# Kernel optimization log

Hardware: AMD Instinct MI355X
Metric: run time of the kernel (lower is better)

Reference implementation:

```python
import jax, jax.numpy as jnp
import numpy as np

N = 131072
K = 1024
D = 64

def setup_inputs() -> dict:
    key = jax.random.key(0)
    k1, k2 = jax.random.split(key)
    x = jax.random.normal(k1, (N, D), dtype=jnp.float32)
    emb_weight = jax.random.normal(k2, (K, D), dtype=jnp.float32)
    return {"x": x, "emb_weight": emb_weight}

def reference(x, emb_weight):
    distances = (
        jnp.sum(x * x, axis=1, keepdims=True)
        + jnp.sum(emb_weight * emb_weight, axis=1)
        - 2.0 * jnp.matmul(x, emb_weight.T)
    )
    codebook_indices = jnp.argmin(distances, axis=1)  # [N]
    probs = jax.nn.one_hot(codebook_indices, K, dtype=x.dtype)  # [N, K]
    z_q = emb_weight[codebook_indices]  # [N, D]
    return (z_q, probs)
```

## Files before the change

kernel.cpp:

```cpp
#include <hip/hip_runtime.h>
#include <math.h>

#define N_TOK 131072
#define K_CB  1024
#define D_DIM 64
#define MARGIN_U 72u

#define WS_EN     0
#define WS_ES     4096
#define WS_CNT    266240
#define WS_LIST   266256

typedef short bf16x8 __attribute__((ext_vector_type(8)));
typedef float f32x4  __attribute__((ext_vector_type(4)));

__device__ __forceinline__ ushort f2bf(float f) {
    uint u = __float_as_uint(f);
    u += 0x7FFFu + ((u >> 16) & 1u);
    return (ushort)(u >> 16);
}
__device__ __forceinline__ float bf2f(ushort h) {
    return __uint_as_float(((uint)h) << 16);
}

__global__ __launch_bounds__(256) void prep_kernel(
    const float* __restrict__ emb, float* __restrict__ en,
    ushort* __restrict__ es, uint* __restrict__ fixcnt)
{
    const int tid = threadIdx.x;
    const int pb  = blockIdx.x;
    const int c6  = tid & 63;
    const int q   = tid >> 6;
    const int code = pb * 64 + c6;
    if (pb == 0 && tid == 0) *fixcnt = 0;

    const int cb = code >> 4, jj = code & 15;
    const float* er = emb + (size_t)code * D_DIM;
    #pragma unroll
    for (int j = 0; j < 16; ++j) {
        int d = q * 16 + j;
        float f = er[d];
        ushort h = f2bf(f);
        ushort l = f2bf(f - bf2f(h));
        int ks = d >> 5, quad = (d >> 3) & 3, e = d & 7;
        es[(size_t)(((cb * 4 + ks)     * 4 + quad) * 16 + jj) * 8 + e] = h;
        es[(size_t)(((cb * 4 + ks + 2) * 4 + quad) * 16 + jj) * 8 + e] = l;
    }
    if (q == 0) {
        float s = 0.f;
        #pragma unroll
        for (int d = 0; d < D_DIM; ++d) s = fmaf(er[d], er[d], s);
        en[code] = s;
    }
}

__global__ __launch_bounds__(256) void vq_onehot(
    const float* __restrict__ x, const float* __restrict__ emb,
    const float* __restrict__ en, const ushort* __restrict__ es,
    float* __restrict__ zq, float* __restrict__ probs,
    uint* __restrict__ fixcnt, uint* __restrict__ fixlist, uint fixcap)
{
    const int tid  = threadIdx.x;
    const int wave = tid >> 6, lane = tid & 63;
    const int quad = lane >> 4, l15 = lane & 15;
    const int rg = wave >> 1;
    const int h  = wave & 1;
    const int blockRow = blockIdx.x * 64;
    const int waveRowBase = blockRow + rg * 32;

    __shared__ uint lds_b1[2][64];
    __shared__ uint lds_b2[2][64];
    __shared__ int  lds_bk[64];

    bf16x8 af[2][4];
    #pragma unroll
    for (int g = 0; g < 2; ++g) {
        const float* xr = x + (size_t)(waveRowBase + g * 16 + l15) * D_DIM + quad * 8;
        f32x4 p0 = *(const f32x4*)(xr);
        f32x4 p1 = *(const f32x4*)(xr + 4);
        f32x4 p2 = *(const f32x4*)(xr + 32);
        f32x4 p3 = *(const f32x4*)(xr + 36);
        float v0[8], v1[8];
        #pragma unroll
        for (int j = 0; j < 4; ++j) { v0[j] = p0[j]; v0[4 + j] = p1[j]; v1[j] = p2[j]; v1[4 + j] = p3[j]; }
        #pragma unroll
        for (int j = 0; j < 8; ++j) {
            ushort h0 = f2bf(v0[j]);
            af[g][0][j] = (short)h0;
            af[g][2][j] = (short)f2bf(v0[j] - bf2f(h0));
            ushort h1 = f2bf(v1[j]);
            af[g][1][j] = (short)h1;
            af[g][3][j] = (short)f2bf(v1[j] - bf2f(h1));
        }
    }

    uint b1u[8], b2u[8];
    #pragma unroll
    for (int s = 0; s < 8; ++s) { b1u[s] = 0xFFFFFFFFu; b2u[s] = 0xFFFFFFFFu; }

    const bf16x8* __restrict__ esv = (const bf16x8*)es;
    const int fidx = quad * 16 + l15;
    const int cb0  = h * 32;

    bf16x8 bc[4]; float enc;
    #pragma unroll
    for (int ks = 0; ks < 4; ++ks) bc[ks] = esv[(size_t)cb0 * 256 + ks * 64 + fidx];
    enc = fmaf(en[cb0 * 16 + l15], 2048.f, 1048576.f);

    const f32x4 zv = {0.f, 0.f, 0.f, 0.f};
    f32x4* pz0 = (f32x4*)probs + (size_t)blockRow * 256 + (size_t)wave * 128 + lane * 2;

    #pragma unroll 2
    for (int i = 0; i < 32; ++i) {
        const int cb  = cb0 + i;
        const int nbi = cb0 + ((i + 1) & 31);
        bf16x8 bn[4]; float enn;
        #pragma unroll
        for (int ks = 0; ks < 4; ++ks) bn[ks] = esv[(size_t)nbi * 256 + ks * 64 + fidx];
        enn = fmaf(en[nbi * 16 + l15], 2048.f, 1048576.f);

        {
            f32x4* pz = pz0 + (size_t)i * 512;
            __builtin_nontemporal_store(zv, pz);
            __builtin_nontemporal_store(zv, pz + 1);
        }

        f32x4 acc0 = {0.f, 0.f, 0.f, 0.f};
        f32x4 acc1 = {0.f, 0.f, 0.f, 0.f};
        acc0 = __builtin_amdgcn_mfma_f32_16x16x32_bf16(af[0][0], bc[0], acc0, 0, 0, 0);
        acc0 = __builtin_amdgcn_mfma_f32_16x16x32_bf16(af[0][1], bc[1], acc0, 0, 0, 0);
        acc0 = __builtin_amdgcn_mfma_f32_16x16x32_bf16(af[0][0], bc[2], acc0, 0, 0, 0);
        acc0 = __builtin_amdgcn_mfma_f32_16x16x32_bf16(af[0][1], bc[3], acc0, 0, 0, 0);
        acc0 = __builtin_amdgcn_mfma_f32_16x16x32_bf16(af[0][2], bc[0], acc0, 0, 0, 0);
        acc0 = __builtin_amdgcn_mfma_f32_16x16x32_bf16(af[0][3], bc[1], acc0, 0, 0, 0);
        acc1 = __builtin_amdgcn_mfma_f32_16x16x32_bf16(af[1][0], bc[0], acc1, 0, 0, 0);
        acc1 = __builtin_amdgcn_mfma_f32_16x16x32_bf16(af[1][1], bc[1], acc1, 0, 0, 0);
        acc1 = __builtin_amdgcn_mfma_f32_16x16x32_bf16(af[1][0], bc[2], acc1, 0, 0, 0);
        acc1 = __builtin_amdgcn_mfma_f32_16x16x32_bf16(af[1][1], bc[3], acc1, 0, 0, 0);
        acc1 = __builtin_amdgcn_mfma_f32_16x16x32_bf16(af[1][2], bc[0], acc1, 0, 0, 0);
        acc1 = __builtin_amdgcn_mfma_f32_16x16x32_bf16(af[1][3], bc[1], acc1, 0, 0, 0);

        const uint code = (uint)(cb * 16 + l15);
        #pragma unroll
        for (int r = 0; r < 4; ++r) {
            {
                float f = fmaf(-4096.f, acc0[r], enc);
                uint u = ((uint)f << 10) | code;
                uint lo = min(b1u[r], u), hi = max(b1u[r], u);
                b1u[r] = lo; b2u[r] = min(b2u[r], hi);
            }
            {
                int s = 4 + r;
                float f = fmaf(-4096.f, acc1[r], enc);
                uint u = ((uint)f << 10) | code;
                uint lo = min(b1u[s], u), hi = max(b1u[s], u);
                b1u[s] = lo; b2u[s] = min(b2u[s], hi);
            }
        }

        #pragma unroll
        for (int ks = 0; ks < 4; ++ks) bc[ks] = bn[ks];
        enc = enn;
    }

    #pragma unroll
    for (int s = 0; s < 8; ++s) {
        #pragma unroll
        for (int off = 1; off < 16; off <<= 1) {
            uint o1 = (uint)__shfl_xor((int)b1u[s], off);
            uint o2 = (uint)__shfl_xor((int)b2u[s], off);
            uint lo = min(b1u[s], o1), hi = max(b1u[s], o1);
            b1u[s] = lo;
            b2u[s] = min(min(b2u[s], o2), hi);
        }
    }

    if (l15 == 0) {
        #pragma unroll
        for (int s = 0; s < 8; ++s) {
            int idx = rg * 32 + (s >> 2) * 16 + quad * 4 + (s & 3);
            lds_b1[h][idx] = b1u[s];
            lds_b2[h][idx] = b2u[s];
        }
    }
    __syncthreads();

    if (tid < 64) {
        uint a1 = lds_b1[0][tid], a2 = lds_b2[0][tid];
        uint c1 = lds_b1[1][tid], c2 = lds_b2[1][tid];
        uint m1 = min(a1, c1);
        uint m2 = min(min(a2, c2), max(a1, c1));
        int  mk = (int)(m1 & 1023u);
        lds_bk[tid] = mk;
        probs[(size_t)(blockRow + tid) * K_CB + mk] = 1.0f;
        if ((m2 >> 10) - (m1 >> 10) <= MARGIN_U) {
            uint idx = atomicAdd(fixcnt, 1u);
            if (idx < fixcap) fixlist[idx] = (uint)(blockRow + tid) | ((uint)mk << 17);
        }
    }
    __syncthreads();

    #pragma unroll
    for (int mb = 0; mb < 4; ++mb) {
        int rl = wave * 16 + mb * 4 + quad;
        int bk = lds_bk[rl];
        f32x4 v = ((const f32x4*)(emb + (size_t)bk * D_DIM))[l15];
        __builtin_nontemporal_store(v, (f32x4*)(zq + (size_t)(blockRow + rl) * D_DIM) + l15);
    }
}

__global__ __launch_bounds__(256) void vq_fixup(
    const float* __restrict__ x, const float* __restrict__ emb,
    const float* __restrict__ en,
    float* __restrict__ zq, float* __restrict__ probs,
    const uint* __restrict__ fixcnt, const uint* __restrict__ fixlist, uint fixcap)
{
    const int lane = threadIdx.x & 63;
    const int quad = lane >> 4, l15 = lane & 15;
    const uint gwave = (uint)((blockIdx.x * 256 + threadIdx.x) >> 6);
    uint cnt = *fixcnt;
    if (cnt > fixcap) cnt = fixcap;

    for (uint e = gwave; e < cnt; e += 4096u) {
        uint w = fixlist[e];
        int row = (int)(w & 0x1FFFFu);
        int kg  = (int)(w >> 17);

        const f32x4* xr4 = (const f32x4*)(x + (size_t)row * D_DIM) + quad * 4;
        f32x4 xv[4];
        #pragma unroll
        for (int c = 0; c < 4; ++c) xv[c] = xr4[c];
        float xn = 0.f;
        #pragma unroll
        for (int c = 0; c < 4; ++c)
            #pragma unroll
            for (int j = 0; j < 4; ++j) xn = fmaf(xv[c][j], xv[c][j], xn);
        xn += __shfl_xor(xn, 16);
        xn += __shfl_xor(xn, 32);

        float bd = INFINITY; int bk = 0;
        #pragma unroll 2
        for (int t = 0; t < 64; ++t) {
            int code = t * 16 + l15;
            const f32x4* er4 = (const f32x4*)(emb + (size_t)code * D_DIM) + quad * 4;
            float dot = 0.f;
            #pragma unroll
            for (int c = 0; c < 4; ++c) {
                f32x4 ev = er4[c];
                #pragma unroll
                for (int j = 0; j < 4; ++j) dot = fmaf(xv[c][j], ev[j], dot);
            }
            dot += __shfl_xor(dot, 16);
            dot += __shfl_xor(dot, 32);
            float dist = fmaf(-2.f, dot, xn + en[code]);
            if (dist < bd) { bd = dist; bk = code; }
        }
        #pragma unroll
        for (int off = 1; off < 16; off <<= 1) {
            float od = __shfl_xor(bd, off);
            int   ok = __shfl_xor(bk, off);
            if (od < bd || (od == bd && ok < bk)) { bd = od; bk = ok; }
        }
        if (bk != kg) {
            if (lane == 0) {
                probs[(size_t)row * K_CB + kg] = 0.f;
                probs[(size_t)row * K_CB + bk] = 1.f;
            }
            if (lane < 16)
                ((f32x4*)(zq + (size_t)row * D_DIM))[lane] =
                    ((const f32x4*)(emb + (size_t)bk * D_DIM))[lane];
        }
    }
}

extern "C" void kernel_launch(void* const* d_in, const int* in_sizes, int n_in,
                              void* d_out, int out_size, void* d_ws, size_t ws_size,
                              hipStream_t stream) {
    const float* x   = (const float*)d_in[0];
    const float* emb = (const float*)d_in[1];
    float* zq    = (float*)d_out;
    float* probs = (float*)d_out + (size_t)N_TOK * D_DIM;

    char* ws = (char*)d_ws;
    float*  en      = (float*)(ws + WS_EN);
    ushort* es      = (ushort*)(ws + WS_ES);
    uint*   fixcnt  = (uint*)(ws + WS_CNT);
    uint*   fixlist = (uint*)(ws + WS_LIST);
    uint fixcap = (ws_size > WS_LIST + 4) ? (uint)((ws_size - WS_LIST) / 4) : 0u;

    prep_kernel<<<16, 256, 0, stream>>>(emb, en, es, fixcnt);
    vq_onehot<<<N_TOK / 64, 256, 0, stream>>>(x, emb, en, es, zq, probs, fixcnt, fixlist, fixcap);
    vq_fixup<<<1024, 256, 0, stream>>>(x, emb, en, zq, probs, fixcnt, fixlist, fixcap);
}
```

Before: 744.7 us.

## Use single bf16 GEMM with norm-scaled fixup margin and fused one-hot row writes

Replaces the split-bf16 (hi+lo) three-pass product with a single bf16 pass, halving the codebook staging and cutting the MFMA count per tile from six to two. To preserve exact argmin, the fixup threshold becomes adaptive, proportional to the row norm of x, which is now computed in the main kernel. The probs row is written whole, with the one-hot value built per vector, instead of zero-fill stores inside the loop followed by a scattered 1.0 store. Prep and fixup launch sizes are adjusted. The main risk is that more rows fall into the exact fixup pass because of the looser bf16 error bound.

```diff
diff --git a/kernel.cpp b/kernel.cpp
--- a/kernel.cpp
+++ b/kernel.cpp
@@ -4,12 +4,11 @@
 #define N_TOK 131072
 #define K_CB  1024
 #define D_DIM 64
-#define MARGIN_U 72u
 
 #define WS_EN     0
 #define WS_ES     4096
-#define WS_CNT    266240
-#define WS_LIST   266256
+#define WS_CNT    135168
+#define WS_LIST   135184
 
 typedef short bf16x8 __attribute__((ext_vector_type(8)));
 typedef float f32x4  __attribute__((ext_vector_type(4)));
@@ -18,9 +17,6 @@
     uint u = __float_as_uint(f);
     u += 0x7FFFu + ((u >> 16) & 1u);
     return (ushort)(u >> 16);
-}
-__device__ __forceinline__ float bf2f(ushort h) {
-    return __uint_as_float(((uint)h) << 16);
 }
 
 __global__ __launch_bounds__(256) void prep_kernel(
@@ -28,29 +24,36 @@
     ushort* __restrict__ es, uint* __restrict__ fixcnt)
 {
     const int tid = threadIdx.x;
-    const int pb  = blockIdx.x;
-    const int c6  = tid & 63;
-    const int q   = tid >> 6;
-    const int code = pb * 64 + c6;
-    if (pb == 0 && tid == 0) *fixcnt = 0;
-
-    const int cb = code >> 4, jj = code & 15;
-    const float* er = emb + (size_t)code * D_DIM;
-    #pragma unroll
-    for (int j = 0; j < 16; ++j) {
-        int d = q * 16 + j;
-        float f = er[d];
-        ushort h = f2bf(f);
-        ushort l = f2bf(f - bf2f(h));
-        int ks = d >> 5, quad = (d >> 3) & 3, e = d & 7;
-        es[(size_t)(((cb * 4 + ks)     * 4 + quad) * 16 + jj) * 8 + e] = h;
-        es[(size_t)(((cb * 4 + ks + 2) * 4 + quad) * 16 + jj) * 8 + e] = l;
-    }
-    if (q == 0) {
+    const int b   = blockIdx.x;
+    if (b == 0 && tid == 0) *fixcnt = 0;
+
+    const int half = tid >> 7;
+    const int t    = tid & 127;
+    const int cb   = b * 2 + half;
+    const int jj   = t & 15;
+    const int quad = (t >> 4) & 3;
+    const int ks   = (t >> 6) & 1;
+    const int code = cb * 16 + jj;
+
+    const float* er = emb + (size_t)code * D_DIM + ks * 32 + quad * 8;
+    f32x4 pa = *(const f32x4*)(er);
+    f32x4 pb = *(const f32x4*)(er + 4);
+
+    bf16x8 hi;
+    #pragma unroll
+    for (int j = 0; j < 8; ++j) {
+        float f = (j < 4) ? pa[j] : pb[j - 4];
+        hi[j] = (short)f2bf(f);
+    }
+    ((bf16x8*)es)[(size_t)(cb * 2 + ks) * 64 + quad * 16 + jj] = hi;
+
+    if (tid < 32) {
+        const int c2 = b * 32 + tid;
+        const float* e2 = emb + (size_t)c2 * D_DIM;
         float s = 0.f;
         #pragma unroll
-        for (int d = 0; d < D_DIM; ++d) s = fmaf(er[d], er[d], s);
-        en[code] = s;
+        for (int d = 0; d < D_DIM; ++d) s = fmaf(e2[d], e2[d], s);
+        en[c2] = s;
     }
 }
 
@@ -68,11 +71,13 @@
     const int blockRow = blockIdx.x * 64;
     const int waveRowBase = blockRow + rg * 32;
 
-    __shared__ uint lds_b1[2][64];
-    __shared__ uint lds_b2[2][64];
-    __shared__ int  lds_bk[64];
-
-    bf16x8 af[2][4];
+    __shared__ uint  lds_b1[2][64];
+    __shared__ uint  lds_b2[2][64];
+    __shared__ int   lds_bk[64];
+    __shared__ float lds_xn[64];
+
+    bf16x8 af[2][2];
+    float xn[2];
     #pragma unroll
     for (int g = 0; g < 2; ++g) {
         const float* xr = x + (size_t)(waveRowBase + g * 16 + l15) * D_DIM + quad * 8;
@@ -83,15 +88,21 @@
         float v0[8], v1[8];
         #pragma unroll
         for (int j = 0; j < 4; ++j) { v0[j] = p0[j]; v0[4 + j] = p1[j]; v1[j] = p2[j]; v1[4 + j] = p3[j]; }
+        float s = 0.f;
         #pragma unroll
         for (int j = 0; j < 8; ++j) {
-            ushort h0 = f2bf(v0[j]);
-            af[g][0][j] = (short)h0;
-            af[g][2][j] = (short)f2bf(v0[j] - bf2f(h0));
-            ushort h1 = f2bf(v1[j]);
-            af[g][1][j] = (short)h1;
-            af[g][3][j] = (short)f2bf(v1[j] - bf2f(h1));
-        }
+            s = fmaf(v0[j], v0[j], s);
+            s = fmaf(v1[j], v1[j], s);
+            af[g][0][j] = (short)f2bf(v0[j]);
+            af[g][1][j] = (short)f2bf(v1[j]);
+        }
+        s += __shfl_xor(s, 16);
+        s += __shfl_xor(s, 32);
+        xn[g] = s;
+    }
+    if (h == 0 && quad == 0) {
+        lds_xn[rg * 32 + l15]      = xn[0];
+        lds_xn[rg * 32 + 16 + l15] = xn[1];
     }
 
     uint b1u[8], b2u[8];
@@ -102,43 +113,26 @@
     const int fidx = quad * 16 + l15;
     const int cb0  = h * 32;
 
-    bf16x8 bc[4]; float enc;
-    #pragma unroll
-    for (int ks = 0; ks < 4; ++ks) bc[ks] = esv[(size_t)cb0 * 256 + ks * 64 + fidx];
-    enc = fmaf(en[cb0 * 16 + l15], 2048.f, 1048576.f);
-
-    const f32x4 zv = {0.f, 0.f, 0.f, 0.f};
-    f32x4* pz0 = (f32x4*)probs + (size_t)blockRow * 256 + (size_t)wave * 128 + lane * 2;
+    bf16x8 bc[2]; float enc;
+    #pragma unroll
+    for (int ks = 0; ks < 2; ++ks) bc[ks] = esv[(size_t)cb0 * 128 + ks * 64 + fidx];
+    enc = fmaf(en[cb0 * 16 + l15], 2048.f, 786432.f);
 
     #pragma unroll 2
     for (int i = 0; i < 32; ++i) {
         const int cb  = cb0 + i;
         const int nbi = cb0 + ((i + 1) & 31);
-        bf16x8 bn[4]; float enn;
-        #pragma unroll
-        for (int ks = 0; ks < 4; ++ks) bn[ks] = esv[(size_t)nbi * 256 + ks * 64 + fidx];
-        enn = fmaf(en[nbi * 16 + l15], 2048.f, 1048576.f);
-
-        {
-            f32x4* pz = pz0 + (size_t)i * 512;
-            __builtin_nontemporal_store(zv, pz);
-            __builtin_nontemporal_store(zv, pz + 1);
-        }
+        bf16x8 bn[2]; float enn;
+        #pragma unroll
+        for (int ks = 0; ks < 2; ++ks) bn[ks] = esv[(size_t)nbi * 128 + ks * 64 + fidx];
+        enn = fmaf(en[nbi * 16 + l15], 2048.f, 786432.f);
 
         f32x4 acc0 = {0.f, 0.f, 0.f, 0.f};
         f32x4 acc1 = {0.f, 0.f, 0.f, 0.f};
         acc0 = __builtin_amdgcn_mfma_f32_16x16x32_bf16(af[0][0], bc[0], acc0, 0, 0, 0);
         acc0 = __builtin_amdgcn_mfma_f32_16x16x32_bf16(af[0][1], bc[1], acc0, 0, 0, 0);
-        acc0 = __builtin_amdgcn_mfma_f32_16x16x32_bf16(af[0][0], bc[2], acc0, 0, 0, 0);
-        acc0 = __builtin_amdgcn_mfma_f32_16x16x32_bf16(af[0][1], bc[3], acc0, 0, 0, 0);
-        acc0 = __builtin_amdgcn_mfma_f32_16x16x32_bf16(af[0][2], bc[0], acc0, 0, 0, 0);
-        acc0 = __builtin_amdgcn_mfma_f32_16x16x32_bf16(af[0][3], bc[1], acc0, 0, 0, 0);
         acc1 = __builtin_amdgcn_mfma_f32_16x16x32_bf16(af[1][0], bc[0], acc1, 0, 0, 0);
         acc1 = __builtin_amdgcn_mfma_f32_16x16x32_bf16(af[1][1], bc[1], acc1, 0, 0, 0);
-        acc1 = __builtin_amdgcn_mfma_f32_16x16x32_bf16(af[1][0], bc[2], acc1, 0, 0, 0);
-        acc1 = __builtin_amdgcn_mfma_f32_16x16x32_bf16(af[1][1], bc[3], acc1, 0, 0, 0);
-        acc1 = __builtin_amdgcn_mfma_f32_16x16x32_bf16(af[1][2], bc[0], acc1, 0, 0, 0);
-        acc1 = __builtin_amdgcn_mfma_f32_16x16x32_bf16(af[1][3], bc[1], acc1, 0, 0, 0);
 
         const uint code = (uint)(cb * 16 + l15);
         #pragma unroll
@@ -159,7 +153,7 @@
         }
 
         #pragma unroll
-        for (int ks = 0; ks < 4; ++ks) bc[ks] = bn[ks];
+        for (int ks = 0; ks < 2; ++ks) bc[ks] = bn[ks];
         enc = enn;
     }
 
@@ -192,8 +186,9 @@
         uint m2 = min(min(a2, c2), max(a1, c1));
         int  mk = (int)(m1 & 1023u);
         lds_bk[tid] = mk;
-        probs[(size_t)(blockRow + tid) * K_CB + mk] = 1.0f;
-        if ((m2 >> 10) - (m1 >> 10) <= MARGIN_U) {
+        uint gap = (m2 >> 10) - (m1 >> 10);
+        uint thr = (uint)(416.0f * sqrtf(lds_xn[tid])) + 4u;
+        if (gap <= thr) {
             uint idx = atomicAdd(fixcnt, 1u);
             if (idx < fixcap) fixlist[idx] = (uint)(blockRow + tid) | ((uint)mk << 17);
         }
@@ -205,7 +200,23 @@
         int rl = wave * 16 + mb * 4 + quad;
         int bk = lds_bk[rl];
         f32x4 v = ((const f32x4*)(emb + (size_t)bk * D_DIM))[l15];
-        __builtin_nontemporal_store(v, (f32x4*)(zq + (size_t)(blockRow + rl) * D_DIM) + l15);
+        ((f32x4*)(zq + (size_t)(blockRow + rl) * D_DIM))[l15] = v;
+    }
+
+    for (int m = 0; m < 16; ++m) {
+        int rl = wave * 16 + m;
+        int bk = lds_bk[rl];
+        float* prow = probs + (size_t)(blockRow + rl) * K_CB;
+        #pragma unroll
+        for (int s = 0; s < 4; ++s) {
+            int c = s * 256 + lane * 4;
+            f32x4 v;
+            v[0] = (c     == bk) ? 1.f : 0.f;
+            v[1] = (c + 1 == bk) ? 1.f : 0.f;
+            v[2] = (c + 2 == bk) ? 1.f : 0.f;
+            v[3] = (c + 3 == bk) ? 1.f : 0.f;
+            *(f32x4*)(prow + c) = v;
+        }
     }
 }
 
@@ -221,7 +232,7 @@
     uint cnt = *fixcnt;
     if (cnt > fixcap) cnt = fixcap;
 
-    for (uint e = gwave; e < cnt; e += 4096u) {
+    for (uint e = gwave; e < cnt; e += 2048u) {
         uint w = fixlist[e];
         int row = (int)(w & 0x1FFFFu);
         int kg  = (int)(w >> 17);
@@ -239,7 +250,6 @@
         xn += __shfl_xor(xn, 32);
 
         float bd = INFINITY; int bk = 0;
-        #pragma unroll 2
         for (int t = 0; t < 64; ++t) {
             int code = t * 16 + l15;
             const f32x4* er4 = (const f32x4*)(emb + (size_t)code * D_DIM) + quad * 4;
@@ -288,7 +298,7 @@
     uint*   fixlist = (uint*)(ws + WS_LIST);
     uint fixcap = (ws_size > WS_LIST + 4) ? (uint)((ws_size - WS_LIST) / 4) : 0u;
 
-    prep_kernel<<<16, 256, 0, stream>>>(emb, en, es, fixcnt);
+    prep_kernel<<<32, 256, 0, stream>>>(emb, en, es, fixcnt);
     vq_onehot<<<N_TOK / 64, 256, 0, stream>>>(x, emb, en, es, zq, probs, fixcnt, fixlist, fixcap);
-    vq_fixup<<<1024, 256, 0, stream>>>(x, emb, en, zq, probs, fixcnt, fixlist, fixcap);
-}
+    vq_fixup<<<512, 256, 0, stream>>>(x, emb, en, zq, probs, fixcnt, fixlist, fixcap);
+}
```

Result: slower. 1.778 ms (+138.8%).
